# Kernel tuning notes

Measured on AMD Instinct MI355X. Metric: run time of the kernel, lower is better.

## Reference

```python
import jax, jax.numpy as jnp
import numpy as np

EMB_DIM = 1024
NUM_HEADS = 16
HEAD_DIM = EMB_DIM // NUM_HEADS


def setup_inputs() -> dict:
    key = jax.random.key(0)
    ks = jax.random.split(key, 6)
    B, S, D = 2, 2048, EMB_DIM
    x = jax.random.normal(ks[0], (B, S, D), dtype=jnp.float32)
    # torch nn.Linear default init: U(-1/sqrt(in), 1/sqrt(in)); weights stored [out,in]
    lim = 1.0 / np.sqrt(D)
    Wq = jax.random.uniform(ks[1], (D, D), jnp.float32, -lim, lim)
    Wk = jax.random.uniform(ks[2], (D, D), jnp.float32, -lim, lim)
    Wv = jax.random.uniform(ks[3], (D, D), jnp.float32, -lim, lim)
    Wo = jax.random.uniform(ks[4], (D, D), jnp.float32, -lim, lim)
    q_scale = jnp.ones((1, 1, D), jnp.float32)
    k_scale = jnp.ones((1, 1, D), jnp.float32)
    v_scale = jnp.ones((1, 1, D), jnp.float32)
    o_scale = jnp.ones((1, 1, D), jnp.float32)
    return {"x": x, "Wq": Wq, "Wk": Wk, "Wv": Wv, "Wo": Wo,
            "q_scale": q_scale, "k_scale": k_scale,
            "v_scale": v_scale, "o_scale": o_scale}


def reference(x, Wq, Wk, Wv, Wo, q_scale, k_scale, v_scale, o_scale):
    B, S, D = x.shape
    H, Hd = NUM_HEADS, HEAD_DIM
    # linear (torch: x @ W^T) then per-channel scale
    Q = (x @ Wq.T) * q_scale
    K = (x @ Wk.T) * k_scale
    V = (x @ Wv.T) * v_scale
    # [B, H, S, Hd]
    Q = Q.reshape(B, S, H, Hd).transpose(0, 2, 1, 3)
    K = K.reshape(B, S, H, Hd).transpose(0, 2, 1, 3)
    V = V.reshape(B, S, H, Hd).transpose(0, 2, 1, 3)
    scores = jnp.einsum("bhqd,bhkd->bhqk", Q, K) / jnp.sqrt(
        jnp.asarray(Hd, jnp.float32))
    probs = jax.nn.softmax(scores, axis=-1)
    ctx = jnp.einsum("bhqk,bhkd->bhqd", probs, V)
    ctx = ctx.transpose(0, 2, 1, 3).reshape(B, S, D)
    return (ctx @ Wo.T) * o_scale
```

## Files before the change

### kernel.cpp

```cpp
#include <hip/hip_runtime.h>
#include <hip/hip_bf16.h>
#include <stdint.h>


typedef __bf16 bf16;
typedef __attribute__((ext_vector_type(8))) __bf16 bf16x8;
typedef __attribute__((ext_vector_type(4))) float f32x4;

#define DEVI __device__ __forceinline__

DEVI void gl_lds16(const void* g, void* l) {
  __builtin_amdgcn_global_load_lds(
      (const __attribute__((address_space(1))) void*)g,
      (__attribute__((address_space(3))) void*)l, 16, 0, 0);
}

DEVI bf16x8 load8(const bf16* p) { return *(const bf16x8*)p; }
DEVI bf16x8 load8(const float* p) {
  f32x4 a = *(const f32x4*)p;
  f32x4 b = *(const f32x4*)(p + 4);
  bf16x8 r;
  r[0] = (bf16)a[0]; r[1] = (bf16)a[1]; r[2] = (bf16)a[2]; r[3] = (bf16)a[3];
  r[4] = (bf16)b[0]; r[5] = (bf16)b[1]; r[6] = (bf16)b[2]; r[7] = (bf16)b[3];
  return r;
}

__global__ __launch_bounds__(256)
void cvt_kernel(const float* __restrict__ x,
                const float* __restrict__ w0, const float* __restrict__ w1,
                const float* __restrict__ w2, const float* __restrict__ w3,
                bf16* __restrict__ xb, bf16* __restrict__ wb) {
  const int y = blockIdx.y;
  const float* src;
  bf16* dst;
  if (y < 4) {
    src = (y == 0) ? w0 : (y == 1) ? w1 : (y == 2) ? w2 : w3;
    dst = wb + (size_t)y * 1048576;
  } else {
    src = x + (size_t)(y - 4) * 1048576;
    dst = xb + (size_t)(y - 4) * 1048576;
  }
  const int i = (blockIdx.x * 256 + threadIdx.x) * 8;
  *(bf16x8*)(dst + i) = load8(src + i);
}

template <typename XT, typename WT, int NTILE>
__global__ __launch_bounds__(256, 2)
void gemm_kernel(const XT* __restrict__ X,
                 const WT* __restrict__ W0, const WT* __restrict__ W1,
                 const WT* __restrict__ W2,
                 const float* __restrict__ s0, const float* __restrict__ s1,
                 const float* __restrict__ s2,
                 bf16* __restrict__ o0, bf16* __restrict__ o1,
                 bf16* __restrict__ o2, float* __restrict__ ofp, int three) {
  constexpr int NF = NTILE / 32;
  constexpr bool ASYNC_A = (sizeof(XT) == 2);
  constexpr bool ASYNC_B = (sizeof(WT) == 2);
  __shared__ bf16 As[128 * 32];
  __shared__ bf16 Bs[NTILE * 32];

  const int t = threadIdx.x;
  const int lane = t & 63;
  const int w = t >> 6;
  const int wm = w >> 1, wn = w & 1;
  const int m0 = blockIdx.x * 128;
  const int cl = lane & 15, quad = lane >> 4;

  const WT* Wp; const float* sp; bf16* op; int mode, n0; float emul = 1.f;
  if (three) {
    int which = blockIdx.y >> 3;
    n0 = (blockIdx.y & 7) * 128;
    if (which == 0)      { Wp = W0; sp = s0; op = o0; mode = 1; emul = 0.18033688f; }
    else if (which == 1) { Wp = W1; sp = s1; op = o1; mode = 1; }
    else                 { Wp = W2; sp = s2; op = o2; mode = 2; }
  } else {
    n0 = blockIdx.y * NTILE; Wp = W0; sp = s0; op = o0; mode = 0;
  }

  f32x4 zero = {0.f, 0.f, 0.f, 0.f};
  f32x4 acc[4][NF];
#pragma unroll
  for (int i = 0; i < 4; i++)
#pragma unroll
    for (int j = 0; j < NF; j++) acc[i][j] = zero;

  const int srow = t >> 2;
  const int clog = (t & 3) ^ (srow & 3);
  const int gcol_sw = clog * 8;
  const int gcol = (t & 3) * 8;
  const int sphys = (((t & 3) ^ (srow & 3)) << 3);

  for (int k0 = 0; k0 < 1024; k0 += 32) {
    bf16x8 a0, a1, b0, b1;
    if constexpr (!ASYNC_A) {
      a0 = load8(&X[(uint64_t)(m0 + srow) * 1024 + k0 + gcol]);
      a1 = load8(&X[(uint64_t)(m0 + 64 + srow) * 1024 + k0 + gcol]);
    }
    if constexpr (!ASYNC_B) {
      b0 = load8(&Wp[(uint64_t)(n0 + srow) * 1024 + k0 + gcol]);
      if constexpr (NTILE == 128)
        b1 = load8(&Wp[(uint64_t)(n0 + 64 + srow) * 1024 + k0 + gcol]);
    }
    __syncthreads();
    if constexpr (ASYNC_A) {
      gl_lds16(X + (uint64_t)(m0 + srow) * 1024 + k0 + gcol_sw, (char*)As + t * 16);
      gl_lds16(X + (uint64_t)(m0 + 64 + srow) * 1024 + k0 + gcol_sw,
               (char*)As + 4096 + t * 16);
    } else {
      *(bf16x8*)&As[srow * 32 + sphys] = a0;
      *(bf16x8*)&As[(64 + srow) * 32 + sphys] = a1;
    }
    if constexpr (ASYNC_B) {
      gl_lds16(Wp + (uint64_t)(n0 + srow) * 1024 + k0 + gcol_sw, (char*)Bs + t * 16);
      if constexpr (NTILE == 128)
        gl_lds16(Wp + (uint64_t)(n0 + 64 + srow) * 1024 + k0 + gcol_sw,
                 (char*)Bs + 4096 + t * 16);
    } else {
      *(bf16x8*)&Bs[srow * 32 + sphys] = b0;
      if constexpr (NTILE == 128)
        *(bf16x8*)&Bs[(64 + srow) * 32 + sphys] = b1;
    }
    __syncthreads();

    bf16x8 af[4], bfr[NF];
#pragma unroll
    for (int mt = 0; mt < 4; mt++) {
      const int row = wm * 64 + mt * 16 + cl;
      af[mt] = *(const bf16x8*)&As[row * 32 + ((quad ^ (cl & 3)) << 3)];
    }
#pragma unroll
    for (int nt = 0; nt < NF; nt++) {
      const int row = wn * (NF * 16) + nt * 16 + cl;
      bfr[nt] = *(const bf16x8*)&Bs[row * 32 + ((quad ^ (cl & 3)) << 3)];
    }
#pragma unroll
    for (int mt = 0; mt < 4; mt++)
#pragma unroll
      for (int nt = 0; nt < NF; nt++)
        acc[mt][nt] = __builtin_amdgcn_mfma_f32_16x16x32_bf16(af[mt], bfr[nt],
                                                              acc[mt][nt], 0, 0, 0);
  }

#pragma unroll
  for (int nt = 0; nt < NF; nt++) {
    const int gn = n0 + wn * (NF * 16) + nt * 16 + cl;
    const float sc = sp[gn] * emul;
#pragma unroll
    for (int mt = 0; mt < 4; mt++) {
      const int gmb = m0 + wm * 64 + mt * 16 + quad * 4;
#pragma unroll
      for (int r = 0; r < 4; r++) {
        const int gm = gmb + r;
        const float v = acc[mt][nt][r] * sc;
        if (mode == 0) {
          ofp[(uint64_t)gm * 1024 + gn] = v;
        } else {
          const int b = gm >> 11, s = gm & 2047;
          const int h = gn >> 6, hd = gn & 63;
          uint64_t addr;
          if (mode == 1) addr = ((uint64_t)(b * 16 + h) * 2048 + s) * 64 + hd;
          else           addr = ((uint64_t)(b * 16 + h) * 64 + hd) * 2048 + s;
          op[addr] = (bf16)v;
        }
      }
    }
  }
}

__global__ __launch_bounds__(256, 1)
void attn_kernel(const bf16* __restrict__ Qw, const bf16* __restrict__ Kw,
                 const bf16* __restrict__ Vtw, bf16* __restrict__ Ctx) {
  __shared__ bf16 Ks[64 * 64];
  __shared__ bf16 Vs[64 * 64];
  __shared__ bf16 Ps[16 * 16 * 64];

  const int t = threadIdx.x, lane = t & 63, w = t >> 6;
  const int cl = lane & 15, quad = lane >> 4;
  const int bh = blockIdx.y;
  const int b = bh >> 4, h = bh & 15;
  const int q0 = blockIdx.x * 256;

  const bf16* Qh = Qw + (uint64_t)bh * 2048 * 64;
  const bf16* Kh = Kw + (uint64_t)bh * 2048 * 64;
  const bf16* Vh = Vtw + (uint64_t)bh * 64 * 2048;

  bf16x8 qf[4][2];
#pragma unroll
  for (int mt = 0; mt < 4; mt++) {
    const int r = q0 + mt * 64 + w * 16 + cl;
    qf[mt][0] = *(const bf16x8*)&Qh[(uint64_t)r * 64 + quad * 8];
    qf[mt][1] = *(const bf16x8*)&Qh[(uint64_t)r * 64 + 32 + quad * 8];
  }

  f32x4 zero = {0.f, 0.f, 0.f, 0.f};
  f32x4 o_acc[4][4];
  float lsum[4][4];
#pragma unroll
  for (int mt = 0; mt < 4; mt++)
#pragma unroll
    for (int i = 0; i < 4; i++) { o_acc[mt][i] = zero; lsum[mt][i] = 0.f; }

  const int srow = t >> 3;
  const int gcol_sw = ((t & 7) ^ (srow & 7)) * 8;

  for (int k0 = 0; k0 < 2048; k0 += 64) {
    __syncthreads();
    gl_lds16(Kh + (uint64_t)(k0 + srow) * 64 + gcol_sw,        (char*)Ks + t * 16);
    gl_lds16(Kh + (uint64_t)(k0 + 32 + srow) * 64 + gcol_sw,   (char*)Ks + 4096 + t * 16);
    gl_lds16(Vh + (uint64_t)srow * 2048 + k0 + gcol_sw,        (char*)Vs + t * 16);
    gl_lds16(Vh + (uint64_t)(32 + srow) * 2048 + k0 + gcol_sw, (char*)Vs + 4096 + t * 16);
    __syncthreads();

    f32x4 sv[4][4];
#pragma unroll
    for (int nt = 0; nt < 4; nt++) {
      const int krow = nt * 16 + cl;
      bf16x8 kf0 = *(const bf16x8*)&Ks[krow * 64 + ((quad ^ (cl & 7)) << 3)];
      bf16x8 kf1 = *(const bf16x8*)&Ks[krow * 64 + (((quad + 4) ^ (cl & 7)) << 3)];
#pragma unroll
      for (int mt = 0; mt < 4; mt++) {
        f32x4 s = __builtin_amdgcn_mfma_f32_16x16x32_bf16(qf[mt][0], kf0, zero, 0, 0, 0);
        s = __builtin_amdgcn_mfma_f32_16x16x32_bf16(qf[mt][1], kf1, s, 0, 0, 0);
        sv[mt][nt] = s;
      }
    }

#pragma unroll
    for (int mt = 0; mt < 4; mt++) {
      bf16* Pm = Ps + (w * 4 + mt) * 1024;
#pragma unroll
      for (int nt = 0; nt < 4; nt++) {
#pragma unroll
        for (int r = 0; r < 4; r++) {
          const float p = __builtin_amdgcn_exp2f(sv[mt][nt][r]);
          lsum[mt][r] += p;
          const int row = quad * 4 + r;
          Pm[row * 64 + ((((nt * 2 + (cl >> 3)) ^ (row & 7)) << 3) | (cl & 7))] =
              (bf16)p;
        }
      }
    }

    bf16x8 pf[4][2];
#pragma unroll
    for (int mt = 0; mt < 4; mt++) {
      const bf16* Pm = Ps + (w * 4 + mt) * 1024;
      pf[mt][0] = *(const bf16x8*)&Pm[cl * 64 + ((quad ^ (cl & 7)) << 3)];
      pf[mt][1] = *(const bf16x8*)&Pm[cl * 64 + (((quad + 4) ^ (cl & 7)) << 3)];
    }
#pragma unroll
    for (int nt = 0; nt < 4; nt++) {
      const int vrow = nt * 16 + cl;
      bf16x8 v0 = *(const bf16x8*)&Vs[vrow * 64 + ((quad ^ (cl & 7)) << 3)];
      bf16x8 v1 = *(const bf16x8*)&Vs[vrow * 64 + (((quad + 4) ^ (cl & 7)) << 3)];
#pragma unroll
      for (int mt = 0; mt < 4; mt++) {
        o_acc[mt][nt] = __builtin_amdgcn_mfma_f32_16x16x32_bf16(pf[mt][0], v0,
                                                                o_acc[mt][nt], 0, 0, 0);
        o_acc[mt][nt] = __builtin_amdgcn_mfma_f32_16x16x32_bf16(pf[mt][1], v1,
                                                                o_acc[mt][nt], 0, 0, 0);
      }
    }
  }

#pragma unroll
  for (int mt = 0; mt < 4; mt++)
#pragma unroll
    for (int r = 0; r < 4; r++) {
      float l = lsum[mt][r];
      l += __shfl_xor(l, 1);
      l += __shfl_xor(l, 2);
      l += __shfl_xor(l, 4);
      l += __shfl_xor(l, 8);
      lsum[mt][r] = 1.0f / l;
    }
#pragma unroll
  for (int mt = 0; mt < 4; mt++)
#pragma unroll
    for (int nt = 0; nt < 4; nt++)
#pragma unroll
      for (int r = 0; r < 4; r++) {
        const int s = q0 + mt * 64 + w * 16 + quad * 4 + r;
        const int hd = nt * 16 + cl;
        Ctx[(uint64_t)(b * 2048 + s) * 1024 + h * 64 + hd] =
            (bf16)(o_acc[mt][nt][r] * lsum[mt][r]);
      }
}

extern "C" void kernel_launch(void* const* d_in, const int* in_sizes, int n_in,
                              void* d_out, int out_size, void* d_ws, size_t ws_size,
                              hipStream_t stream) {
  const float* x  = (const float*)d_in[0];
  const float* Wq = (const float*)d_in[1];
  const float* Wk = (const float*)d_in[2];
  const float* Wv = (const float*)d_in[3];
  const float* Wo = (const float*)d_in[4];
  const float* qs = (const float*)d_in[5];
  const float* ks = (const float*)d_in[6];
  const float* vs = (const float*)d_in[7];
  const float* os = (const float*)d_in[8];
  float* out = (float*)d_out;

  const size_t M4 = 4194304, M1 = 1048576;

  if (ws_size >= (size_t)40 * 1024 * 1024) {
    bf16* xb = (bf16*)d_ws;
    bf16* wb = xb + M4;
    bf16* qw = wb + M4;
    bf16* kw = qw + M4;
    bf16* vw = kw + M4;
    bf16* cw = xb;

    cvt_kernel<<<dim3(512, 8), 256, 0, stream>>>(x, Wq, Wk, Wv, Wo, xb, wb);
    gemm_kernel<bf16, bf16, 128><<<dim3(32, 24), 256, 0, stream>>>(
        xb, wb, wb + M1, wb + 2 * M1, qs, ks, vs, qw, kw, vw, nullptr, 1);
    attn_kernel<<<dim3(8, 32), 256, 0, stream>>>(qw, kw, vw, cw);
    gemm_kernel<bf16, bf16, 64><<<dim3(32, 16), 256, 0, stream>>>(
        cw, wb + 3 * M1, nullptr, nullptr, os, nullptr, nullptr,
        nullptr, nullptr, nullptr, out, 0);
  } else {
    bf16* qw = (bf16*)d_ws;
    bf16* kw = qw + M4;
    bf16* vw = kw + M4;
    bf16* cw = vw + M4;
    gemm_kernel<float, float, 128><<<dim3(32, 24), 256, 0, stream>>>(
        x, Wq, Wk, Wv, qs, ks, vs, qw, kw, vw, nullptr, 1);
    attn_kernel<<<dim3(8, 32), 256, 0, stream>>>(qw, kw, vw, cw);
    gemm_kernel<bf16, float, 64><<<dim3(32, 16), 256, 0, stream>>>(
        cw, Wo, nullptr, nullptr, os, nullptr, nullptr,
        nullptr, nullptr, nullptr, out, 0);
  }
}
```

Measured before the change: 221.1 us.

## Halve attention query tile, compute transposed scores, pack P stores

Each attention block now covers 128 queries instead of 256, so the grid doubles to 16x32 and launch bounds allow two blocks per CU. The QK^T MFMA is issued with swapped operands, which yields transposed score fragments. Each thread can then write four packed bf16 probabilities as one vector LDS store with a new XOR swizzle, instead of scalar stores, and the row-sum reduction becomes cross-quad shuffles plus a broadcast. The aim is better latency hiding, fewer LDS store instructions and less register pressure, at the cost of loading K/V tiles twice as often per head.

After: 194.9 us. -11.8%, faster.

```diff
diff --git a/kernel.cpp b/kernel.cpp
--- a/kernel.cpp
+++ b/kernel.cpp
@@ -5,6 +5,7 @@
 
 typedef __bf16 bf16;
 typedef __attribute__((ext_vector_type(8))) __bf16 bf16x8;
+typedef __attribute__((ext_vector_type(4))) __bf16 bf16x4;
 typedef __attribute__((ext_vector_type(4))) float f32x4;
 
 #define DEVI __device__ __forceinline__
@@ -85,8 +86,7 @@
     for (int j = 0; j < NF; j++) acc[i][j] = zero;
 
   const int srow = t >> 2;
-  const int clog = (t & 3) ^ (srow & 3);
-  const int gcol_sw = clog * 8;
+  const int gcol_sw = ((t & 3) ^ (srow & 3)) * 8;
   const int gcol = (t & 3) * 8;
   const int sphys = (((t & 3) ^ (srow & 3)) << 3);
 
@@ -167,41 +167,42 @@
   }
 }
 
-__global__ __launch_bounds__(256, 1)
+__global__ __launch_bounds__(256, 2)
 void attn_kernel(const bf16* __restrict__ Qw, const bf16* __restrict__ Kw,
                  const bf16* __restrict__ Vtw, bf16* __restrict__ Ctx) {
   __shared__ bf16 Ks[64 * 64];
   __shared__ bf16 Vs[64 * 64];
-  __shared__ bf16 Ps[16 * 16 * 64];
+  __shared__ bf16 Ps[8 * 16 * 64];
 
   const int t = threadIdx.x, lane = t & 63, w = t >> 6;
   const int cl = lane & 15, quad = lane >> 4;
   const int bh = blockIdx.y;
   const int b = bh >> 4, h = bh & 15;
-  const int q0 = blockIdx.x * 256;
+  const int q0 = blockIdx.x * 128;
 
   const bf16* Qh = Qw + (uint64_t)bh * 2048 * 64;
   const bf16* Kh = Kw + (uint64_t)bh * 2048 * 64;
   const bf16* Vh = Vtw + (uint64_t)bh * 64 * 2048;
 
-  bf16x8 qf[4][2];
-#pragma unroll
-  for (int mt = 0; mt < 4; mt++) {
+  bf16x8 qf[2][2];
+#pragma unroll
+  for (int mt = 0; mt < 2; mt++) {
     const int r = q0 + mt * 64 + w * 16 + cl;
     qf[mt][0] = *(const bf16x8*)&Qh[(uint64_t)r * 64 + quad * 8];
     qf[mt][1] = *(const bf16x8*)&Qh[(uint64_t)r * 64 + 32 + quad * 8];
   }
 
   f32x4 zero = {0.f, 0.f, 0.f, 0.f};
-  f32x4 o_acc[4][4];
-  float lsum[4][4];
-#pragma unroll
-  for (int mt = 0; mt < 4; mt++)
-#pragma unroll
-    for (int i = 0; i < 4; i++) { o_acc[mt][i] = zero; lsum[mt][i] = 0.f; }
+  f32x4 o_acc[2][4];
+  float lsum[2] = {0.f, 0.f};
+#pragma unroll
+  for (int mt = 0; mt < 2; mt++)
+#pragma unroll
+    for (int i = 0; i < 4; i++) o_acc[mt][i] = zero;
 
   const int srow = t >> 3;
   const int gcol_sw = ((t & 7) ^ (srow & 7)) * 8;
+  const int psw = (cl & 7) << 1;
 
   for (int k0 = 0; k0 < 2048; k0 += 64) {
     __syncthreads();
@@ -211,50 +212,48 @@
     gl_lds16(Vh + (uint64_t)(32 + srow) * 2048 + k0 + gcol_sw, (char*)Vs + 4096 + t * 16);
     __syncthreads();
 
-    f32x4 sv[4][4];
 #pragma unroll
     for (int nt = 0; nt < 4; nt++) {
       const int krow = nt * 16 + cl;
       bf16x8 kf0 = *(const bf16x8*)&Ks[krow * 64 + ((quad ^ (cl & 7)) << 3)];
       bf16x8 kf1 = *(const bf16x8*)&Ks[krow * 64 + (((quad + 4) ^ (cl & 7)) << 3)];
 #pragma unroll
-      for (int mt = 0; mt < 4; mt++) {
-        f32x4 s = __builtin_amdgcn_mfma_f32_16x16x32_bf16(qf[mt][0], kf0, zero, 0, 0, 0);
-        s = __builtin_amdgcn_mfma_f32_16x16x32_bf16(qf[mt][1], kf1, s, 0, 0, 0);
-        sv[mt][nt] = s;
-      }
-    }
-
-#pragma unroll
-    for (int mt = 0; mt < 4; mt++) {
-      bf16* Pm = Ps + (w * 4 + mt) * 1024;
-#pragma unroll
-      for (int nt = 0; nt < 4; nt++) {
+      for (int mt = 0; mt < 2; mt++) {
+        f32x4 s = __builtin_amdgcn_mfma_f32_16x16x32_bf16(kf0, qf[mt][0], zero, 0, 0, 0);
+        s = __builtin_amdgcn_mfma_f32_16x16x32_bf16(kf1, qf[mt][1], s, 0, 0, 0);
+        bf16x4 pk;
+        float ls = 0.f;
 #pragma unroll
         for (int r = 0; r < 4; r++) {
-          const float p = __builtin_amdgcn_exp2f(sv[mt][nt][r]);
-          lsum[mt][r] += p;
-          const int row = quad * 4 + r;
-          Pm[row * 64 + ((((nt * 2 + (cl >> 3)) ^ (row & 7)) << 3) | (cl & 7))] =
-              (bf16)p;
+          const float p = __builtin_amdgcn_exp2f(s[r]);
+          ls += p;
+          pk[r] = (bf16)p;
         }
-      }
-    }
-
-    bf16x8 pf[4][2];
-#pragma unroll
-    for (int mt = 0; mt < 4; mt++) {
-      const bf16* Pm = Ps + (w * 4 + mt) * 1024;
-      pf[mt][0] = *(const bf16x8*)&Pm[cl * 64 + ((quad ^ (cl & 7)) << 3)];
-      pf[mt][1] = *(const bf16x8*)&Pm[cl * 64 + (((quad + 4) ^ (cl & 7)) << 3)];
-    }
+        lsum[mt] += ls;
+        bf16* Pm = Ps + (w * 2 + mt) * 1024;
+        const int c = 4 * nt + quad;
+        *(bf16x4*)&Pm[cl * 64 + ((c ^ psw) << 2)] = pk;
+      }
+    }
+
+    bf16x8 pf[2][2];
+#pragma unroll
+    for (int mt = 0; mt < 2; mt++) {
+      const bf16* Pm = Ps + (w * 2 + mt) * 1024;
+#pragma unroll
+      for (int hh = 0; hh < 2; hh++) {
+        const int c0 = 8 * hh + 2 * quad;
+        pf[mt][hh] = *(const bf16x8*)&Pm[cl * 64 + ((c0 ^ psw) << 2)];
+      }
+    }
+
 #pragma unroll
     for (int nt = 0; nt < 4; nt++) {
       const int vrow = nt * 16 + cl;
       bf16x8 v0 = *(const bf16x8*)&Vs[vrow * 64 + ((quad ^ (cl & 7)) << 3)];
       bf16x8 v1 = *(const bf16x8*)&Vs[vrow * 64 + (((quad + 4) ^ (cl & 7)) << 3)];
 #pragma unroll
-      for (int mt = 0; mt < 4; mt++) {
+      for (int mt = 0; mt < 2; mt++) {
         o_acc[mt][nt] = __builtin_amdgcn_mfma_f32_16x16x32_bf16(pf[mt][0], v0,
                                                                 o_acc[mt][nt], 0, 0, 0);
         o_acc[mt][nt] = __builtin_amdgcn_mfma_f32_16x16x32_bf16(pf[mt][1], v1,
@@ -263,19 +262,20 @@
     }
   }
 
-#pragma unroll
-  for (int mt = 0; mt < 4; mt++)
-#pragma unroll
-    for (int r = 0; r < 4; r++) {
-      float l = lsum[mt][r];
-      l += __shfl_xor(l, 1);
-      l += __shfl_xor(l, 2);
-      l += __shfl_xor(l, 4);
-      l += __shfl_xor(l, 8);
-      lsum[mt][r] = 1.0f / l;
-    }
-#pragma unroll
-  for (int mt = 0; mt < 4; mt++)
+  float linv[2][4];
+#pragma unroll
+  for (int mt = 0; mt < 2; mt++) {
+    float l = lsum[mt];
+    l += __shfl_xor(l, 16);
+    l += __shfl_xor(l, 32);
+    const float inv = 1.0f;
+    (void)inv;
+#pragma unroll
+    for (int r = 0; r < 4; r++)
+      linv[mt][r] = 1.0f / __shfl(l, quad * 4 + r);
+  }
+#pragma unroll
+  for (int mt = 0; mt < 2; mt++)
 #pragma unroll
     for (int nt = 0; nt < 4; nt++)
 #pragma unroll
@@ -283,7 +283,7 @@
         const int s = q0 + mt * 64 + w * 16 + quad * 4 + r;
         const int hd = nt * 16 + cl;
         Ctx[(uint64_t)(b * 2048 + s) * 1024 + h * 64 + hd] =
-            (bf16)(o_acc[mt][nt][r] * lsum[mt][r]);
+            (bf16)(o_acc[mt][nt][r] * linv[mt][r]);
       }
 }
 
@@ -314,7 +314,7 @@
     cvt_kernel<<<dim3(512, 8), 256, 0, stream>>>(x, Wq, Wk, Wv, Wo, xb, wb);
     gemm_kernel<bf16, bf16, 128><<<dim3(32, 24), 256, 0, stream>>>(
         xb, wb, wb + M1, wb + 2 * M1, qs, ks, vs, qw, kw, vw, nullptr, 1);
-    attn_kernel<<<dim3(8, 32), 256, 0, stream>>>(qw, kw, vw, cw);
+    attn_kernel<<<dim3(16, 32), 256, 0, stream>>>(qw, kw, vw, cw);
     gemm_kernel<bf16, bf16, 64><<<dim3(32, 16), 256, 0, stream>>>(
         cw, wb + 3 * M1, nullptr, nullptr, os, nullptr, nullptr,
         nullptr, nullptr, nullptr, out, 0);
@@ -325,7 +325,7 @@
     bf16* cw = vw + M4;
     gemm_kernel<float, float, 128><<<dim3(32, 24), 256, 0, stream>>>(
         x, Wq, Wk, Wv, qs, ks, vs, qw, kw, vw, nullptr, 1);
-    attn_kernel<<<dim3(8, 32), 256, 0, stream>>>(qw, kw, vw, cw);
+    attn_kernel<<<dim3(16, 32), 256, 0, stream>>>(qw, kw, vw, cw);
     gemm_kernel<bf16, float, 64><<<dim3(32, 16), 256, 0, stream>>>(
         cw, Wo, nullptr, nullptr, os, nullptr, nullptr,
         nullptr, nullptr, nullptr, out, 0);
```
